# Kernel optimization log

Measured on AMD Instinct MI355X. Metric: run time of the kernel, lower is better.

The kernel has to match this reference:

```python
import jax, jax.numpy as jnp
import numpy as np

B, T, H, LAT, ADIM = 8192, 40, 100, 10, 2
ATT_TEMP = 5.0


def setup_inputs() -> dict:
    key = jax.random.key(0)
    ks = jax.random.split(key, 12)
    return {
        "sampled_att_z": jax.random.normal(ks[0], (B, LAT), jnp.float32),
        "enc_h": jax.random.normal(ks[1], (B, H), jnp.float32),
        # keep IDM params strictly positive / physically plausible to avoid inf
        "idm_params": 1.0 + 2.0 * jax.random.uniform(ks[2], (B, 5), jnp.float32),
        "idm_s": jax.random.uniform(ks[3], (B, T, 8), jnp.float32),
        "sdv_acts": jax.random.normal(ks[4], (B, T, ADIM), jnp.float32),
        "linear_W": jax.random.normal(ks[5], (LAT, H), jnp.float32) / np.float32(np.sqrt(LAT)),
        "linear_b": jnp.zeros((H,), jnp.float32),
        "lstm_Wx": jax.random.normal(ks[6], (H + ADIM, 4 * H), jnp.float32) / np.float32(np.sqrt(H + ADIM)),
        "lstm_Wh": jax.random.normal(ks[7], (H, 4 * H), jnp.float32) / np.float32(np.sqrt(H)),
        "lstm_b": jnp.zeros((4 * H,), jnp.float32),
        "att_W": jax.random.normal(ks[8], (H, 1), jnp.float32) / np.float32(np.sqrt(H)),
        "att_b": jnp.zeros((1,), jnp.float32),
        # precomputed per-step noise, replacing tf.random.normal inside the loop
        "noise_f": jax.random.normal(ks[9], (T, B, 1), jnp.float32),
        "noise_m": jax.random.normal(ks[10], (T, B, 1), jnp.float32),
    }


def reference(sampled_att_z, enc_h, idm_params, idm_s, sdv_acts,
              linear_W, linear_b, lstm_Wx, lstm_Wh, lstm_b, att_W, att_b,
              noise_f, noise_m):
    desired_v = idm_params[:, 0:1]
    desired_tgap = idm_params[:, 1:2]
    min_jamx = idm_params[:, 2:3]
    max_act = idm_params[:, 3:4]
    min_act = idm_params[:, 4:5]

    def idm_driver(vel, dv, dx):  # all [B,1]
        dx = jnp.clip(dx, 0.5, 1000.0)
        desired_gap = min_jamx + jax.nn.relu(
            desired_tgap * vel + vel * dv / (2.0 * jnp.sqrt(max_act * min_act)))
        act = max_act * (1.0 - (vel / desired_v) ** 4 - (desired_gap / dx) ** 2)
        return jnp.clip(act, -3.0, 3.0)

    att_proj = sampled_att_z @ linear_W + linear_b  # [B,H]; also the att_context and init h,c

    s_tm = jnp.swapaxes(idm_s, 0, 1)      # [T,B,8]
    a_tm = jnp.swapaxes(sdv_acts, 0, 1)   # [T,B,ADIM]

    ego_v0 = idm_s[:, 0, 0:1]
    ego_x0 = idm_s[:, 0, 3:4]
    zero_act = jnp.zeros_like(ego_v0)  # step-0 kinematic update is a no-op

    def step(carry, xs):
        ego_v, ego_x, h, c, act = carry
        s, sdv, nf, nm = xs
        ego_v = ego_v + act * 0.1
        ego_x = ego_x + ego_v * 0.1 + 0.5 * act * 0.1 ** 2

        f_v, m_v = s[:, 1:2], s[:, 2:3]
        f_x, m_x = s[:, 4:5], s[:, 5:6]
        f_ex, m_ex = s[:, 6:7], s[:, 7:8]

        ef_act = idm_driver(ego_v, ego_v - f_v, f_x - ego_x)
        ef_act = f_ex * ef_act + (1.0 - f_ex) * nf
        em_act = idm_driver(ego_v, ego_v - m_v, m_x - ego_x)
        em_act = m_ex * em_act + (1.0 - m_ex) * nm

        x_in = jnp.concatenate([att_proj, sdv], axis=-1)  # [B,H+ADIM]
        z = x_in @ lstm_Wx + h @ lstm_Wh + lstm_b          # [B,4H], keras gate order i,f,g,o
        zi, zf, zg, zo = jnp.split(z, 4, axis=-1)
        c = jax.nn.sigmoid(zf) * c + jax.nn.sigmoid(zi) * jnp.tanh(zg)
        h = jax.nn.sigmoid(zo) * jnp.tanh(c)

        att_score = jax.nn.sigmoid(ATT_TEMP * (h @ att_W + att_b))  # [B,1]
        act = (1.0 - att_score) * ef_act + att_score * em_act
        return (ego_v, ego_x, h, c, act), (act, att_score)

    init = (ego_v0, ego_x0, att_proj, att_proj, zero_act)
    _, (acts, atts) = jax.lax.scan(step, init, (s_tm, a_tm, noise_f, noise_m))
    act_seq = jnp.swapaxes(acts, 0, 1)  # [B,T,1]
    att_seq = jnp.swapaxes(atts, 0, 1)  # [B,T,1]
    return act_seq, att_seq
```

## Files before the change

kernel.cpp:

```cpp
#include <hip/hip_runtime.h>
#include <math.h>


#define B_TOT 8192
#define T_STEPS 40
#define NB 16

typedef _Float16 f16;
typedef f16 f16x4 __attribute__((ext_vector_type(4)));
typedef f16 f16x8 __attribute__((ext_vector_type(8)));
typedef float f32x4 __attribute__((ext_vector_type(4)));

__device__ __forceinline__ float rcpf(float x) { return __builtin_amdgcn_rcpf(x); }
__device__ __forceinline__ float ex2(float x)  { return __builtin_amdgcn_exp2f(x); }
__device__ __forceinline__ float sigf(float x)  { return rcpf(1.f + ex2(-1.44269504f * x)); }


__global__ __launch_bounds__(256) void idm_prep(
    const float* __restrict__ Wx, const float* __restrict__ Wh,
    const float* __restrict__ bvec, const float* __restrict__ attw,
    f16* __restrict__ whb, f16* __restrict__ wxb,
    float* __restrict__ bp)
{
  int i = blockIdx.x * 256 + threadIdx.x;
  int k = i >> 9, n = i & 511;
  int g = n >> 7, j128 = n & 127;
  float vh = 0.f, vx = 0.f;
  if (j128 < 100) {
    int col = g * 100 + j128;
    if (k < 100)      { vh = Wh[k * 400 + col]; vx = Wx[k * 400 + col]; }
    else if (k < 102) { vh = Wx[k * 400 + col]; }
  } else if (n == 100 && k < 100) {
    vh = attw[k];
  }
  int idx = (((n >> 4) * 4 + (k >> 5)) * 64 + (((k >> 3) & 3) * 16 + (n & 15))) * 8 + (k & 7);
  whb[idx] = (f16)vh;
  wxb[idx] = (f16)vx;
  if (i < 512) { int gg = i >> 7, jj = i & 127; bp[i] = (jj < 100) ? bvec[gg * 100 + jj] : 0.f; }
}

__global__ __launch_bounds__(448, 4) void idm_main(
    const float* __restrict__ z_att,
    const float* __restrict__ linear_W,
    const float* __restrict__ linear_b,
    const float* __restrict__ sdv_acts,
    const f16* __restrict__ whb, const f16* __restrict__ wxb,
    const float* __restrict__ bp,
    const float* __restrict__ idm_params,
    const float* __restrict__ idm_s,
    const float* __restrict__ att_b,
    const float* __restrict__ noise_f,
    const float* __restrict__ noise_m,
    float* __restrict__ out)
{
  __shared__ f16   hS[2][16][136];
  __shared__ f16   sdvS[T_STEPS][16][2];
  __shared__ float logitS[T_STEPS][16];
  __shared__ float sS[16][T_STEPS][6];
  __shared__ float nS[2][T_STEPS][16];
  __shared__ float accS[2][16][T_STEPS];

  const int tid = threadIdx.x;
  const int w  = tid >> 6;
  const int l  = tid & 63;
  const int lr = l & 15;
  const int lq = l >> 4;
  const int b0g = blockIdx.x * NB;
  const int j0 = 16 * w + lq * 4;

  for (int idx = tid; idx < 2176; idx += 448) ((unsigned*)hS)[idx] = 0u;
  for (int idx = tid; idx < 1280; idx += 448) {
    float v = sdv_acts[(size_t)b0g * 80 + idx];
    int b = idx / 80, r = idx - b * 80;
    sdvS[r >> 1][b][r & 1] = (f16)v;
  }
  for (int idx = tid; idx < 5120; idx += 448) {
    int f = idx & 7;
    if (f != 0 && f != 3) {
      int b = idx / 320, rem = idx - b * 320, t = rem >> 3;
      sS[b][t][(f < 3) ? f - 1 : f - 2] = idm_s[(size_t)b0g * 320 + idx];
    }
  }
  for (int idx = tid; idx < 1280; idx += 448) {
    int which = idx >= 640 ? 1 : 0;
    int r = idx - which * 640;
    int t = r >> 4, i = r & 15;
    nS[which][t][i] = which ? noise_m[(size_t)t * B_TOT + b0g + i]
                            : noise_f[(size_t)t * B_TOT + b0g + i];
  }
  __syncthreads();

  if (tid < 256) {
    int b = tid >> 4, oct = tid & 15;
    float za[10];
    #pragma unroll
    for (int t2 = 0; t2 < 10; ++t2) za[t2] = z_att[(b0g + b) * 10 + t2];
    #pragma unroll
    for (int jj = 0; jj < 8; ++jj) {
      int j = oct * 8 + jj;
      if (j < 100) {
        float acc = linear_b[j];
        #pragma unroll
        for (int t2 = 0; t2 < 10; ++t2) acc = fmaf(za[t2], linear_W[t2 * 100 + j], acc);
        hS[0][b][j] = (f16)acc;
      }
    }
  }
  if (tid < 32) hS[0][tid >> 1][100 + (tid & 1)] = sdvS[0][tid >> 1][tid & 1];
  __syncthreads();

  f16x8 wb[4][4];
  #pragma unroll
  for (int g = 0; g < 4; ++g) {
    int tile = w + 8 * g;
    #pragma unroll
    for (int kf = 0; kf < 4; ++kf)
      wb[g][kf] = *(const f16x8*)(wxb + ((size_t)(tile * 4 + kf) * 64 + l) * 8);
  }
  f32x4 cx[4];
  #pragma unroll
  for (int g = 0; g < 4; ++g)
    cx[g] = *(const f32x4*)(bp + (w + 8 * g) * 16 + lq * 4);
  #pragma unroll
  for (int kf = 0; kf < 4; ++kf) {
    f16x8 a = *(const f16x8*)(&hS[0][lr][kf * 32 + lq * 8]);
    #pragma unroll
    for (int g = 0; g < 4; ++g)
      cx[g] = __builtin_amdgcn_mfma_f32_16x16x32_f16(wb[g][kf], a, cx[g], 0, 0, 0);
  }
  #pragma unroll
  for (int g = 0; g < 4; ++g) {
    int tile = w + 8 * g;
    #pragma unroll
    for (int kf = 0; kf < 4; ++kf)
      wb[g][kf] = *(const f16x8*)(whb + ((size_t)(tile * 4 + kf) * 64 + l) * 8);
  }

  float cst[4];
  #pragma unroll
  for (int r = 0; r < 4; ++r) cst[r] = (float)hS[0][lr][j0 + r];

  const bool hlive = (j0 < 100);
  const bool sduty = (w == 6) && (lq == 1 || lq == 2);
  const int sb = (lq - 1) * 16 + lr;

  int p = 0;
  for (int t = 0; t < T_STEPS; ++t) {
    f16x8 a0 = *(const f16x8*)(&hS[p][lr][0  + lq * 8]);
    f16x8 a1 = *(const f16x8*)(&hS[p][lr][32 + lq * 8]);
    f16x8 a2 = *(const f16x8*)(&hS[p][lr][64 + lq * 8]);
    f16x8 a3 = *(const f16x8*)(&hS[p][lr][96 + lq * 8]);
    f32x4 z0 = cx[0], z1 = cx[1], z2 = cx[2], z3 = cx[3];
    z0 = __builtin_amdgcn_mfma_f32_16x16x32_f16(wb[0][0], a0, z0, 0, 0, 0);
    z1 = __builtin_amdgcn_mfma_f32_16x16x32_f16(wb[1][0], a0, z1, 0, 0, 0);
    z2 = __builtin_amdgcn_mfma_f32_16x16x32_f16(wb[2][0], a0, z2, 0, 0, 0);
    z3 = __builtin_amdgcn_mfma_f32_16x16x32_f16(wb[3][0], a0, z3, 0, 0, 0);
    z0 = __builtin_amdgcn_mfma_f32_16x16x32_f16(wb[0][1], a1, z0, 0, 0, 0);
    z1 = __builtin_amdgcn_mfma_f32_16x16x32_f16(wb[1][1], a1, z1, 0, 0, 0);
    z2 = __builtin_amdgcn_mfma_f32_16x16x32_f16(wb[2][1], a1, z2, 0, 0, 0);
    z3 = __builtin_amdgcn_mfma_f32_16x16x32_f16(wb[3][1], a1, z3, 0, 0, 0);
    z0 = __builtin_amdgcn_mfma_f32_16x16x32_f16(wb[0][2], a2, z0, 0, 0, 0);
    z1 = __builtin_amdgcn_mfma_f32_16x16x32_f16(wb[1][2], a2, z1, 0, 0, 0);
    z2 = __builtin_amdgcn_mfma_f32_16x16x32_f16(wb[2][2], a2, z2, 0, 0, 0);
    z3 = __builtin_amdgcn_mfma_f32_16x16x32_f16(wb[3][2], a2, z3, 0, 0, 0);
    z0 = __builtin_amdgcn_mfma_f32_16x16x32_f16(wb[0][3], a3, z0, 0, 0, 0);
    z1 = __builtin_amdgcn_mfma_f32_16x16x32_f16(wb[1][3], a3, z1, 0, 0, 0);
    z2 = __builtin_amdgcn_mfma_f32_16x16x32_f16(wb[2][3], a3, z2, 0, 0, 0);
    z3 = __builtin_amdgcn_mfma_f32_16x16x32_f16(wb[3][3], a3, z3, 0, 0, 0);

    if (w == 6 && lq == 1 && t > 0) logitS[t - 1][lr] = z0[0];

    f16x4 h4;
    #pragma unroll
    for (int r = 0; r < 4; ++r) {
      float ei = ex2(-1.44269504f * z0[r]);
      float sf = sigf(z1[r]);
      float eg = ex2(-2.88539008f * fmaxf(z2[r], -30.f));
      float it = (1.f - eg) * rcpf((1.f + ei) * (1.f + eg));
      float cc = fmaf(sf, cst[r], it);
      float eo = ex2(-1.44269504f * z3[r]);
      float ec = ex2(-2.88539008f * fmaxf(cc, -30.f));
      float hh = (1.f - ec) * rcpf((1.f + eo) * (1.f + ec));
      cst[r] = cc;
      h4[r] = (f16)hh;
    }
    if (hlive) *(f16x4*)(&hS[p ^ 1][lr][j0]) = h4;
    if (sduty && t + 1 < T_STEPS)
      hS[p ^ 1][sb >> 1][100 + (sb & 1)] = sdvS[t + 1][sb >> 1][sb & 1];
    __syncthreads();
    p ^= 1;
  }

  if (w == 6) {
    f32x4 zL = {0.f, 0.f, 0.f, 0.f};
    #pragma unroll
    for (int kf = 0; kf < 4; ++kf) {
      f16x8 a = *(const f16x8*)(&hS[p][lr][kf * 32 + lq * 8]);
      zL = __builtin_amdgcn_mfma_f32_16x16x32_f16(wb[0][kf], a, zL, 0, 0, 0);
    }
    if (lq == 1) logitS[T_STEPS - 1][lr] = zL[0];
  }
  __syncthreads();

  if (tid < 16) {
    int b = b0g + tid;
    const float* P = idm_params + (size_t)b * 5;
    float des_v = P[0], des_tg = P[1], min_jx = P[2], max_a = P[3];
    float inv2s = 0.5f / sqrtf(max_a * P[4]);
    float inv_dv = rcpf(des_v);
    float ego_v = idm_s[(size_t)b * 320 + 0];
    float ego_x = idm_s[(size_t)b * 320 + 3];
    float attb = att_b[0];
    float act = 0.f;
    #pragma unroll 4
    for (int t = 0; t < T_STEPS; ++t) {
      float2 s01 = *(const float2*)&sS[tid][t][0];
      float2 s23 = *(const float2*)&sS[tid][t][2];
      float2 s45 = *(const float2*)&sS[tid][t][4];
      float nf = nS[0][t][tid], nm = nS[1][t][tid];
      float lg = attb + logitS[t][tid];
      ego_v += act * 0.1f;
      ego_x += ego_v * 0.1f + act * 0.005f;
      float af_, am_;
      {
        float dx = fminf(fmaxf(s23.x - ego_x, 0.5f), 1000.f);
        float dg = min_jx + fmaxf(0.f, des_tg * ego_v + ego_v * (ego_v - s01.x) * inv2s);
        float r = ego_v * inv_dv; float r2 = r * r; float q = dg * rcpf(dx);
        af_ = fminf(fmaxf(max_a * (1.f - r2 * r2 - q * q), -3.f), 3.f);
      }
      {
        float dx = fminf(fmaxf(s23.y - ego_x, 0.5f), 1000.f);
        float dg = min_jx + fmaxf(0.f, des_tg * ego_v + ego_v * (ego_v - s01.y) * inv2s);
        float r = ego_v * inv_dv; float r2 = r * r; float q = dg * rcpf(dx);
        am_ = fminf(fmaxf(max_a * (1.f - r2 * r2 - q * q), -3.f), 3.f);
      }
      float ef2 = s45.x * af_ + (1.f - s45.x) * nf;
      float em2 = s45.y * am_ + (1.f - s45.y) * nm;
      float att = sigf(5.f * lg);
      act = (1.f - att) * ef2 + att * em2;
      accS[0][tid][t] = act;
      accS[1][tid][t] = att;
    }
  }
  __syncthreads();

  if (tid < 160) {
    f32x4 va = ((const f32x4*)&accS[0][0][0])[tid];
    f32x4 vt = ((const f32x4*)&accS[1][0][0])[tid];
    *(f32x4*)(out + (size_t)b0g * T_STEPS + tid * 4) = va;
    *(f32x4*)(out + (size_t)B_TOT * T_STEPS + (size_t)b0g * T_STEPS + tid * 4) = vt;
  }
}

extern "C" void kernel_launch(void* const* d_in, const int* in_sizes, int n_in,
                              void* d_out, int out_size, void* d_ws, size_t ws_size,
                              hipStream_t stream) {
  const float* z_att      = (const float*)d_in[0];
  const float* idm_params = (const float*)d_in[2];
  const float* idm_s      = (const float*)d_in[3];
  const float* sdv_acts   = (const float*)d_in[4];
  const float* linear_W   = (const float*)d_in[5];
  const float* linear_b   = (const float*)d_in[6];
  const float* lstm_Wx    = (const float*)d_in[7];
  const float* lstm_Wh    = (const float*)d_in[8];
  const float* lstm_b     = (const float*)d_in[9];
  const float* att_W      = (const float*)d_in[10];
  const float* att_b      = (const float*)d_in[11];
  const float* noise_f    = (const float*)d_in[12];
  const float* noise_m    = (const float*)d_in[13];
  float* out = (float*)d_out;

  f16*   whb = (f16*)d_ws;
  f16*   wxb = (f16*)((char*)d_ws + 131072);
  float* bp  = (float*)((char*)d_ws + 262144);

  idm_prep<<<256, 256, 0, stream>>>(lstm_Wx, lstm_Wh, lstm_b, att_W, whb, wxb, bp);
  idm_main<<<B_TOT / NB, 448, 0, stream>>>(z_att, linear_W, linear_b, sdv_acts,
                                           whb, wxb, bp,
                                           idm_params, idm_s, att_b,
                                           noise_f, noise_m, out);
}
```

Measured before the change: 184.1 us.

## Interleave two 16-row batch groups per block to overlap MFMA with gate math

Each block now handles 32 batch rows split into two independent LSTM groups, A and B. The recurrence is skewed so that one group's matmul for a step is issued while the other group's gate activations are computed, which hides MFMA latency behind transcendental ALU work. There are now two barriers per step instead of one, but each covers half the work. The cost is more registers (launch bounds lowered to 2 blocks), more LDS per block, and half as many blocks.

```diff
diff --git a/kernel.cpp b/kernel.cpp
--- a/kernel.cpp
+++ b/kernel.cpp
@@ -4,7 +4,6 @@
 
 #define B_TOT 8192
 #define T_STEPS 40
-#define NB 16
 
 typedef _Float16 f16;
 typedef f16 f16x4 __attribute__((ext_vector_type(4)));
@@ -39,7 +38,26 @@
   if (i < 512) { int gg = i >> 7, jj = i & 127; bp[i] = (jj < 100) ? bvec[gg * 100 + jj] : 0.f; }
 }
 
-__global__ __launch_bounds__(448, 4) void idm_main(
+#define GATES(ZS, CST, DEST)                                            \
+  {                                                                     \
+    f16x4 h4;                                                           \
+    _Pragma("unroll")                                                   \
+    for (int r = 0; r < 4; ++r) {                                       \
+      float ei = ex2(-1.44269504f * ZS[0][r]);                          \
+      float sf = sigf(ZS[1][r]);                                        \
+      float eg = ex2(-2.88539008f * fmaxf(ZS[2][r], -30.f));            \
+      float it = (1.f - eg) * rcpf((1.f + ei) * (1.f + eg));            \
+      float cc = fmaf(sf, CST[r], it);                                  \
+      float eo = ex2(-1.44269504f * ZS[3][r]);                          \
+      float ec = ex2(-2.88539008f * fmaxf(cc, -30.f));                  \
+      float hh = (1.f - ec) * rcpf((1.f + eo) * (1.f + ec));            \
+      CST[r] = cc;                                                      \
+      h4[r] = (f16)hh;                                                  \
+    }                                                                   \
+    if (hlive) *(f16x4*)(&DEST[lr][j0]) = h4;                           \
+  }
+
+__global__ __launch_bounds__(448, 2) void idm_main(
     const float* __restrict__ z_att,
     const float* __restrict__ linear_W,
     const float* __restrict__ linear_b,
@@ -53,60 +71,71 @@
     const float* __restrict__ noise_m,
     float* __restrict__ out)
 {
-  __shared__ f16   hS[2][16][136];
-  __shared__ f16   sdvS[T_STEPS][16][2];
-  __shared__ float logitS[T_STEPS][16];
-  __shared__ float sS[16][T_STEPS][6];
-  __shared__ float nS[2][T_STEPS][16];
-  __shared__ float accS[2][16][T_STEPS];
+  __shared__ f16   hA[16][136], hB[16][136];
+  __shared__ f16   sdvS[T_STEPS][32][2];
+  __shared__ float logitS[T_STEPS][32];
+  __shared__ float sS[32][T_STEPS][6];
+  __shared__ float nS[2][T_STEPS][32];
+  __shared__ float accS[2][32][T_STEPS];
 
   const int tid = threadIdx.x;
   const int w  = tid >> 6;
   const int l  = tid & 63;
   const int lr = l & 15;
   const int lq = l >> 4;
-  const int b0g = blockIdx.x * NB;
+  const int b0g = blockIdx.x * 32;
   const int j0 = 16 * w + lq * 4;
-
-  for (int idx = tid; idx < 2176; idx += 448) ((unsigned*)hS)[idx] = 0u;
-  for (int idx = tid; idx < 1280; idx += 448) {
+  const bool hlive = (j0 < 100);
+  const bool w6log = (w == 6 && lq == 1);
+  const bool sduty = (w == 6 && (lq == 1 || lq == 2));
+
+  for (int idx = tid; idx < 1088; idx += 448) {
+    ((unsigned*)hA)[idx] = 0u; ((unsigned*)hB)[idx] = 0u;
+  }
+  for (int idx = tid; idx < 2560; idx += 448) {
     float v = sdv_acts[(size_t)b0g * 80 + idx];
     int b = idx / 80, r = idx - b * 80;
     sdvS[r >> 1][b][r & 1] = (f16)v;
   }
-  for (int idx = tid; idx < 5120; idx += 448) {
+  for (int idx = tid; idx < 10240; idx += 448) {
     int f = idx & 7;
     if (f != 0 && f != 3) {
       int b = idx / 320, rem = idx - b * 320, t = rem >> 3;
       sS[b][t][(f < 3) ? f - 1 : f - 2] = idm_s[(size_t)b0g * 320 + idx];
     }
   }
-  for (int idx = tid; idx < 1280; idx += 448) {
-    int which = idx >= 640 ? 1 : 0;
-    int r = idx - which * 640;
-    int t = r >> 4, i = r & 15;
+  for (int idx = tid; idx < 2560; idx += 448) {
+    int which = idx >= 1280 ? 1 : 0;
+    int r = idx - which * 1280;
+    int t = r >> 5, i = r & 31;
     nS[which][t][i] = which ? noise_m[(size_t)t * B_TOT + b0g + i]
                             : noise_f[(size_t)t * B_TOT + b0g + i];
   }
   __syncthreads();
 
-  if (tid < 256) {
-    int b = tid >> 4, oct = tid & 15;
-    float za[10];
-    #pragma unroll
-    for (int t2 = 0; t2 < 10; ++t2) za[t2] = z_att[(b0g + b) * 10 + t2];
-    #pragma unroll
-    for (int jj = 0; jj < 8; ++jj) {
-      int j = oct * 8 + jj;
-      if (j < 100) {
-        float acc = linear_b[j];
-        #pragma unroll
-        for (int t2 = 0; t2 < 10; ++t2) acc = fmaf(za[t2], linear_W[t2 * 100 + j], acc);
-        hS[0][b][j] = (f16)acc;
+  #pragma unroll
+  for (int grp = 0; grp < 2; ++grp) {
+    if (tid < 256) {
+      int b = tid >> 4, oct = tid & 15;
+      float za[10];
+      #pragma unroll
+      for (int t2 = 0; t2 < 10; ++t2) za[t2] = z_att[(b0g + grp * 16 + b) * 10 + t2];
+      #pragma unroll
+      for (int jj = 0; jj < 8; ++jj) {
+        int j = oct * 8 + jj;
+        if (j < 100) {
+          float acc = linear_b[j];
+          #pragma unroll
+          for (int t2 = 0; t2 < 10; ++t2) acc = fmaf(za[t2], linear_W[t2 * 100 + j], acc);
+          (grp ? hB : hA)[b][j] = (f16)acc;
+        }
       }
     }
   }
-  if (tid < 32) hS[0][tid >> 1][100 + (tid & 1)] = sdvS[0][tid >> 1][tid & 1];
+  if (tid < 64) {
+    int b = tid >> 1, ii = tid & 1;
+    (b >= 16 ? hB : hA)[b & 15][100 + ii] = sdvS[0][b][ii];
+  }
   __syncthreads();
 
   f16x8 wb[4][4];
@@ -117,16 +146,21 @@
     for (int kf = 0; kf < 4; ++kf)
       wb[g][kf] = *(const f16x8*)(wxb + ((size_t)(tile * 4 + kf) * 64 + l) * 8);
   }
-  f32x4 cx[4];
-  #pragma unroll
-  for (int g = 0; g < 4; ++g)
-    cx[g] = *(const f32x4*)(bp + (w + 8 * g) * 16 + lq * 4);
+  f32x4 cxA[4], cxB[4];
+  #pragma unroll
+  for (int g = 0; g < 4; ++g) {
+    f32x4 bv = *(const f32x4*)(bp + (w + 8 * g) * 16 + lq * 4);
+    cxA[g] = bv; cxB[g] = bv;
+  }
   #pragma unroll
   for (int kf = 0; kf < 4; ++kf) {
-    f16x8 a = *(const f16x8*)(&hS[0][lr][kf * 32 + lq * 8]);
-    #pragma unroll
-    for (int g = 0; g < 4; ++g)
-      cx[g] = __builtin_amdgcn_mfma_f32_16x16x32_f16(wb[g][kf], a, cx[g], 0, 0, 0);
+    f16x8 aA = *(const f16x8*)(&hA[lr][kf * 32 + lq * 8]);
+    f16x8 aB = *(const f16x8*)(&hB[lr][kf * 32 + lq * 8]);
+    #pragma unroll
+    for (int g = 0; g < 4; ++g) {
+      cxA[g] = __builtin_amdgcn_mfma_f32_16x16x32_f16(wb[g][kf], aA, cxA[g], 0, 0, 0);
+      cxB[g] = __builtin_amdgcn_mfma_f32_16x16x32_f16(wb[g][kf], aB, cxB[g], 0, 0, 0);
+    }
   }
   #pragma unroll
   for (int g = 0; g < 4; ++g) {
@@ -136,73 +170,66 @@
       wb[g][kf] = *(const f16x8*)(whb + ((size_t)(tile * 4 + kf) * 64 + l) * 8);
   }
 
-  float cst[4];
-  #pragma unroll
-  for (int r = 0; r < 4; ++r) cst[r] = (float)hS[0][lr][j0 + r];
-
-  const bool hlive = (j0 < 100);
-  const bool sduty = (w == 6) && (lq == 1 || lq == 2);
-  const int sb = (lq - 1) * 16 + lr;
-
-  int p = 0;
+  f32x4 zB[4] = {cxB[0], cxB[1], cxB[2], cxB[3]};
+  #pragma unroll
+  for (int kf = 0; kf < 4; ++kf) {
+    f16x8 aB = *(const f16x8*)(&hB[lr][kf * 32 + lq * 8]);
+    #pragma unroll
+    for (int g = 0; g < 4; ++g)
+      zB[g] = __builtin_amdgcn_mfma_f32_16x16x32_f16(wb[g][kf], aB, zB[g], 0, 0, 0);
+  }
+  float cstA[4], cstB[4];
+  #pragma unroll
+  for (int r = 0; r < 4; ++r) {
+    cstA[r] = (float)hA[lr][j0 + r];
+    cstB[r] = (float)hB[lr][j0 + r];
+  }
+  __syncthreads();
+
   for (int t = 0; t < T_STEPS; ++t) {
-    f16x8 a0 = *(const f16x8*)(&hS[p][lr][0  + lq * 8]);
-    f16x8 a1 = *(const f16x8*)(&hS[p][lr][32 + lq * 8]);
-    f16x8 a2 = *(const f16x8*)(&hS[p][lr][64 + lq * 8]);
-    f16x8 a3 = *(const f16x8*)(&hS[p][lr][96 + lq * 8]);
-    f32x4 z0 = cx[0], z1 = cx[1], z2 = cx[2], z3 = cx[3];
-    z0 = __builtin_amdgcn_mfma_f32_16x16x32_f16(wb[0][0], a0, z0, 0, 0, 0);
-    z1 = __builtin_amdgcn_mfma_f32_16x16x32_f16(wb[1][0], a0, z1, 0, 0, 0);
-    z2 = __builtin_amdgcn_mfma_f32_16x16x32_f16(wb[2][0], a0, z2, 0, 0, 0);
-    z3 = __builtin_amdgcn_mfma_f32_16x16x32_f16(wb[3][0], a0, z3, 0, 0, 0);
-    z0 = __builtin_amdgcn_mfma_f32_16x16x32_f16(wb[0][1], a1, z0, 0, 0, 0);
-    z1 = __builtin_amdgcn_mfma_f32_16x16x32_f16(wb[1][1], a1, z1, 0, 0, 0);
-    z2 = __builtin_amdgcn_mfma_f32_16x16x32_f16(wb[2][1], a1, z2, 0, 0, 0);
-    z3 = __builtin_amdgcn_mfma_f32_16x16x32_f16(wb[3][1], a1, z3, 0, 0, 0);
-    z0 = __builtin_amdgcn_mfma_f32_16x16x32_f16(wb[0][2], a2, z0, 0, 0, 0);
-    z1 = __builtin_amdgcn_mfma_f32_16x16x32_f16(wb[1][2], a2, z1, 0, 0, 0);
-    z2 = __builtin_amdgcn_mfma_f32_16x16x32_f16(wb[2][2], a2, z2, 0, 0, 0);
-    z3 = __builtin_amdgcn_mfma_f32_16x16x32_f16(wb[3][2], a2, z3, 0, 0, 0);
-    z0 = __builtin_amdgcn_mfma_f32_16x16x32_f16(wb[0][3], a3, z0, 0, 0, 0);
-    z1 = __builtin_amdgcn_mfma_f32_16x16x32_f16(wb[1][3], a3, z1, 0, 0, 0);
-    z2 = __builtin_amdgcn_mfma_f32_16x16x32_f16(wb[2][3], a3, z2, 0, 0, 0);
-    z3 = __builtin_amdgcn_mfma_f32_16x16x32_f16(wb[3][3], a3, z3, 0, 0, 0);
-
-    if (w == 6 && lq == 1 && t > 0) logitS[t - 1][lr] = z0[0];
-
-    f16x4 h4;
-    #pragma unroll
-    for (int r = 0; r < 4; ++r) {
-      float ei = ex2(-1.44269504f * z0[r]);
-      float sf = sigf(z1[r]);
-      float eg = ex2(-2.88539008f * fmaxf(z2[r], -30.f));
-      float it = (1.f - eg) * rcpf((1.f + ei) * (1.f + eg));
-      float cc = fmaf(sf, cst[r], it);
-      float eo = ex2(-1.44269504f * z3[r]);
-      float ec = ex2(-2.88539008f * fmaxf(cc, -30.f));
-      float hh = (1.f - ec) * rcpf((1.f + eo) * (1.f + ec));
-      cst[r] = cc;
-      h4[r] = (f16)hh;
-    }
-    if (hlive) *(f16x4*)(&hS[p ^ 1][lr][j0]) = h4;
+    f32x4 zA[4] = {cxA[0], cxA[1], cxA[2], cxA[3]};
+    #pragma unroll
+    for (int kf = 0; kf < 4; ++kf) {
+      f16x8 a = *(const f16x8*)(&hA[lr][kf * 32 + lq * 8]);
+      #pragma unroll
+      for (int g = 0; g < 4; ++g)
+        zA[g] = __builtin_amdgcn_mfma_f32_16x16x32_f16(wb[g][kf], a, zA[g], 0, 0, 0);
+    }
+    if (w6log && t > 0) logitS[t - 1][16 + lr] = zB[0][0];
+    GATES(zB, cstB, hB)
     if (sduty && t + 1 < T_STEPS)
-      hS[p ^ 1][sb >> 1][100 + (sb & 1)] = sdvS[t + 1][sb >> 1][sb & 1];
+      hB[lr][100 + (lq - 1)] = sdvS[t + 1][16 + lr][lq - 1];
     __syncthreads();
-    p ^= 1;
-  }
-
+
+    if (w6log && t > 0) logitS[t - 1][lr] = zA[0][0];
+    #pragma unroll
+    for (int g = 0; g < 4; ++g) zB[g] = cxB[g];
+    #pragma unroll
+    for (int kf = 0; kf < 4; ++kf) {
+      f16x8 a = *(const f16x8*)(&hB[lr][kf * 32 + lq * 8]);
+      #pragma unroll
+      for (int g = 0; g < 4; ++g)
+        zB[g] = __builtin_amdgcn_mfma_f32_16x16x32_f16(wb[g][kf], a, zB[g], 0, 0, 0);
+    }
+    GATES(zA, cstA, hA)
+    if (sduty && t + 1 < T_STEPS)
+      hA[lr][100 + (lq - 1)] = sdvS[t + 1][lr][lq - 1];
+    __syncthreads();
+  }
+
+  if (w6log) logitS[T_STEPS - 1][16 + lr] = zB[0][0];
   if (w == 6) {
     f32x4 zL = {0.f, 0.f, 0.f, 0.f};
     #pragma unroll
     for (int kf = 0; kf < 4; ++kf) {
-      f16x8 a = *(const f16x8*)(&hS[p][lr][kf * 32 + lq * 8]);
+      f16x8 a = *(const f16x8*)(&hA[lr][kf * 32 + lq * 8]);
       zL = __builtin_amdgcn_mfma_f32_16x16x32_f16(wb[0][kf], a, zL, 0, 0, 0);
     }
     if (lq == 1) logitS[T_STEPS - 1][lr] = zL[0];
   }
   __syncthreads();
 
-  if (tid < 16) {
+  if (tid < 32) {
     int b = b0g + tid;
     const float* P = idm_params + (size_t)b * 5;
     float des_v = P[0], des_tg = P[1], min_jx = P[2], max_a = P[3];
@@ -244,7 +271,7 @@
   }
   __syncthreads();
 
-  if (tid < 160) {
+  if (tid < 320) {
     f32x4 va = ((const f32x4*)&accS[0][0][0])[tid];
     f32x4 vt = ((const f32x4*)&accS[1][0][0])[tid];
     *(f32x4*)(out + (size_t)b0g * T_STEPS + tid * 4) = va;
@@ -275,7 +302,7 @@
   float* bp  = (float*)((char*)d_ws + 262144);
 
   idm_prep<<<256, 256, 0, stream>>>(lstm_Wx, lstm_Wh, lstm_b, att_W, whb, wxb, bp);
-  idm_main<<<B_TOT / NB, 448, 0, stream>>>(z_att, linear_W, linear_b, sdv_acts,
+  idm_main<<<B_TOT / 32, 448, 0, stream>>>(z_att, linear_W, linear_b, sdv_acts,
                                            whb, wxb, bp,
                                            idm_params, idm_s, att_b,
                                            noise_f, noise_m, out);
```

After: 188.4 us. +2.3%, slower.
